# Kernel optimization log

Measured on AMD Instinct MI355X. Metric: run time of the kernel, lower is better.

Reference implementation:

```python
import jax, jax.numpy as jnp
import numpy as np


def setup_inputs() -> dict:
    key = jax.random.key(0)
    ks = jax.random.split(key, 5)
    b, l, ns, ni, d = 128, 64, 32, 16, 256
    scale = 1.0 / np.sqrt(d)
    return {
        "token_features": jax.random.normal(ks[0], (b, l, d), jnp.float32),
        "w_route_ws": jax.random.normal(ks[1], (l, ns, d), jnp.float32) * scale,
        "w_pose_ws": jax.random.normal(ks[2], (l, ns, d, d), jnp.float32) * scale,
        "w_route_si": jax.random.normal(ks[3], (ns, ni, d), jnp.float32) * scale,
        "w_pose_si": jax.random.normal(ks[4], (ns, ni, d, d), jnp.float32) * scale,
    }


def reference(token_features, w_route_ws, w_pose_ws, w_route_si, w_pose_si):
    d_model = token_features.shape[-1]

    # ---- route words -> slots ----
    # token activations ('norm' strategy): mean over d_model -> (b, l)
    a_words = jnp.sum(token_features, axis=-1) / d_model
    # routing logits (b, l, n_slot_caps), softmax over slot caps
    c_ws = jax.nn.softmax(jnp.einsum('lnj,blj->bln', w_route_ws, token_features), axis=-1)
    weighted_c = jnp.einsum('bls,bl->bs', c_ws, a_words)            # (b, ns)
    a_slots = weighted_c / jnp.sum(a_words, axis=-1, keepdims=True)  # (b, ns)
    # pose votes (b, l, ns, d) then weighted aggregation + divisive normalization
    u_hat_slots = jnp.einsum('lnij,blj->blni', w_pose_ws, token_features)
    u_slots = jnp.einsum('bls,bl,blsk->bsk', c_ws, a_words, u_hat_slots) / weighted_c[:, :, None]

    # ---- route slots -> intents ----
    c_si = jax.nn.softmax(jnp.einsum('sij,bsj->bsi', w_route_si, u_slots), axis=-1)
    weighted_c2 = jnp.einsum('bsi,bs->bi', c_si, a_slots)            # (b, ni)
    a_intents = weighted_c2 / jnp.sum(a_slots, axis=-1, keepdims=True)
    u_hat_intents = jnp.einsum('sijk,bsk->bsik', w_pose_si, u_slots)  # (b, ns, ni, d)
    u_intents = jnp.einsum('bsi,bs,bsik->bik', c_si, a_slots, u_hat_intents) / weighted_c2[:, :, None]

    return a_slots, u_slots, a_intents, u_intents
```

## Files before the change

### kernel.cpp

```cpp
#include <hip/hip_runtime.h>
#include <math.h>

#define B  128
#define L  64
#define NS 32
#define NI 16
#define D  256

typedef __attribute__((ext_vector_type(8))) short bf16x8;
typedef __attribute__((ext_vector_type(4))) float f32x4;

__device__ __forceinline__ float wave_reduce_sum(float v) {
#pragma unroll
  for (int off = 32; off; off >>= 1) v += __shfl_xor(v, off, 64);
  return v;
}
__device__ __forceinline__ float wave_reduce_max(float v) {
#pragma unroll
  for (int off = 32; off; off >>= 1) v = fmaxf(v, __shfl_xor(v, off, 64));
  return v;
}

__device__ __forceinline__ ushort bf16_rtne(float f) {
  unsigned u = __float_as_uint(f);
  unsigned r = 0x7FFFu + ((u >> 16) & 1u);
  return (ushort)((u + r) >> 16);
}
__device__ __forceinline__ void split2(float x, ushort& hi, ushort& lo) {
  ushort h = bf16_rtne(x);
  float hf = __uint_as_float(((unsigned)h) << 16);
  hi = h;
  lo = bf16_rtne(x - hf);
}

__global__ __launch_bounds__(256) void k1_route_words(
    const float* __restrict__ tf, const float* __restrict__ wr,
    float* __restrict__ wls, float* __restrict__ a_words) {
  int bl = blockIdx.x;
  int l  = bl & (L - 1);
  int t  = threadIdx.x;
  int wave = t >> 6, lane = t & 63;
  __shared__ float sx[D];
  __shared__ float slog[NS];
  __shared__ float s_aw;
  sx[t] = tf[bl * D + t];
  __syncthreads();
  const float* wbase = wr + l * NS * D;
#pragma unroll
  for (int r = 0; r < 8; ++r) {
    int n = wave * 8 + r;
    const float* w = wbase + n * D;
    float p = 0.f;
#pragma unroll
    for (int jj = 0; jj < 4; ++jj) {
      int j = lane + jj * 64;
      p = fmaf(w[j], sx[j], p);
    }
    p = wave_reduce_sum(p);
    if (lane == 0) slog[n] = p;
  }
  if (wave == 0) {
    float p = sx[lane] + sx[lane + 64] + sx[lane + 128] + sx[lane + 192];
    p = wave_reduce_sum(p);
    if (lane == 0) s_aw = p * (1.f / D);
  }
  __syncthreads();
  if (wave == 0) {
    float aw = s_aw;
    float v = (lane < NS) ? slog[lane] : -INFINITY;
    float m = wave_reduce_max(v);
    float e = (lane < NS) ? __expf(v - m) : 0.f;
    float s = wave_reduce_sum(e);
    if (lane < NS) wls[bl * NS + lane] = (e / s) * aw;
    if (lane == 0) a_words[bl] = aw;
  }
}

__global__ __launch_bounds__(64) void k2_slots_agg(
    const float* __restrict__ wls, const float* __restrict__ a_words,
    float* __restrict__ weighted_c, float* __restrict__ a_slots) {
  int b = blockIdx.x;
  int lane = threadIdx.x;
  float aw = a_words[b * L + lane];
  float sa = wave_reduce_sum(aw);
  if (lane < NS) {
    float wc = 0.f;
    for (int l = 0; l < L; ++l) wc += wls[(b * L + l) * NS + lane];
    weighted_c[b * NS + lane] = wc;
    a_slots[b * NS + lane] = wc / sa;
  }
}

#define BM 128
#define BN 128
#define KC 64
#define KP 72

__global__ __launch_bounds__(256) void k3_mfma(
    const float* __restrict__ tf, const float* __restrict__ wp,
    const float* __restrict__ wls, float* __restrict__ part, int nsplit) {
  __shared__ ushort Ah[BM][KP], Al[BM][KP], Wh[BN][KP], Wl[BN][KP];
  __shared__ float sw[BM];

  int bx   = blockIdx.x;
  int sp   = bx % nsplit;
  int rest = bx / nsplit;
  int it   = rest & 1;
  int s    = rest >> 1;
  int i0   = it * BN;
  int lchunk = L / nsplit;
  int l0     = sp * lchunk;

  int t    = threadIdx.x;
  int jq   = (t & 15) * 4;
  int rb   = t >> 4;
  int lane = t & 63;
  int w    = t >> 6;
  int wm   = w >> 1, wn = w & 1;
  int arow = wm * 64 + (lane & 15);
  int brow = wn * 64 + (lane & 15);
  int ko   = (lane >> 4) * 8;

  f32x4 acc[4][4];
#pragma unroll
  for (int i = 0; i < 4; ++i)
#pragma unroll
    for (int j = 0; j < 4; ++j) acc[i][j] = (f32x4)0.f;

  for (int li = 0; li < lchunk; ++li) {
    int l = l0 + li;
    __syncthreads();
    if (t < BM) sw[t] = wls[((size_t)t * L + l) * NS + s];
    __syncthreads();
    const float* wbase = wp + (size_t)(l * NS + s) * (D * D);
    for (int jc = 0; jc < D; jc += KC) {
      if (jc) __syncthreads();
#pragma unroll
      for (int p = 0; p < 8; ++p) {
        int bb = p * 16 + rb;
        const float4 v = *(const float4*)(tf + ((size_t)bb * L + l) * D + jc + jq);
        float sc = sw[bb];
        ushort4 h4, l4;
        split2(v.x * sc, h4.x, l4.x);
        split2(v.y * sc, h4.y, l4.y);
        split2(v.z * sc, h4.z, l4.z);
        split2(v.w * sc, h4.w, l4.w);
        *(ushort4*)&Ah[bb][jq] = h4;
        *(ushort4*)&Al[bb][jq] = l4;
      }
#pragma unroll
      for (int p = 0; p < 8; ++p) {
        int ii = p * 16 + rb;
        const float4 v = *(const float4*)(wbase + (size_t)(i0 + ii) * D + jc + jq);
        ushort4 h4, l4;
        split2(v.x, h4.x, l4.x);
        split2(v.y, h4.y, l4.y);
        split2(v.z, h4.z, l4.z);
        split2(v.w, h4.w, l4.w);
        *(ushort4*)&Wh[ii][jq] = h4;
        *(ushort4*)&Wl[ii][jq] = l4;
      }
      __syncthreads();
#pragma unroll
      for (int k32 = 0; k32 < 2; ++k32) {
        int kb = k32 * 32 + ko;
        bf16x8 ah[4], av[4], bh[4], bv[4];
#pragma unroll
        for (int mi = 0; mi < 4; ++mi) {
          ah[mi] = *(const bf16x8*)&Ah[arow + mi * 16][kb];
          av[mi] = *(const bf16x8*)&Al[arow + mi * 16][kb];
        }
#pragma unroll
        for (int ni = 0; ni < 4; ++ni) {
          bh[ni] = *(const bf16x8*)&Wh[brow + ni * 16][kb];
          bv[ni] = *(const bf16x8*)&Wl[brow + ni * 16][kb];
        }
#pragma unroll
        for (int mi = 0; mi < 4; ++mi)
#pragma unroll
          for (int ni = 0; ni < 4; ++ni) {
            acc[mi][ni] = __builtin_amdgcn_mfma_f32_16x16x32_bf16(
                ah[mi], bh[ni], acc[mi][ni], 0, 0, 0);
            acc[mi][ni] = __builtin_amdgcn_mfma_f32_16x16x32_bf16(
                ah[mi], bv[ni], acc[mi][ni], 0, 0, 0);
            acc[mi][ni] = __builtin_amdgcn_mfma_f32_16x16x32_bf16(
                av[mi], bh[ni], acc[mi][ni], 0, 0, 0);
          }
      }
    }
  }
  float* pout = part + (((size_t)sp * NS + s) * B) * D + i0;
#pragma unroll
  for (int mi = 0; mi < 4; ++mi)
#pragma unroll
    for (int ni = 0; ni < 4; ++ni) {
      int col = wn * 64 + ni * 16 + (lane & 15);
#pragma unroll
      for (int r = 0; r < 4; ++r) {
        int bb = wm * 64 + mi * 16 + (lane >> 4) * 4 + r;
        pout[(size_t)bb * D + col] = acc[mi][ni][r];
      }
    }
}

__global__ __launch_bounds__(256) void k3r_reduce(
    const float* __restrict__ part, const float* __restrict__ wc,
    float* __restrict__ u_slots, int nsplit) {
  int idx = blockIdx.x * 256 + threadIdx.x;
  int i  = idx & (D - 1);
  int sb = idx >> 8;
  int b  = sb & (B - 1);
  int s  = sb >> 7;
  float v = 0.f;
  for (int sp = 0; sp < nsplit; ++sp)
    v += part[(size_t)sp * (NS * B * D) + idx];
  u_slots[((size_t)b * NS + s) * D + i] = v / wc[b * NS + s];
}

__global__ __launch_bounds__(64) void k4_route_si(
    const float* __restrict__ u_slots, const float* __restrict__ wr_si,
    const float* __restrict__ a_slots, float* __restrict__ w2) {
  int bs = blockIdx.x;
  int s  = bs & (NS - 1);
  int lane = threadIdx.x;
  __shared__ float su[D];
  __shared__ float slog[NI];
#pragma unroll
  for (int jj = 0; jj < 4; ++jj) su[lane + jj * 64] = u_slots[bs * D + lane + jj * 64];
  __syncthreads();
  for (int i = 0; i < NI; ++i) {
    const float* w = wr_si + (s * NI + i) * D;
    float p = 0.f;
#pragma unroll
    for (int jj = 0; jj < 4; ++jj) {
      int j = lane + jj * 64;
      p = fmaf(w[j], su[j], p);
    }
    p = wave_reduce_sum(p);
    if (lane == 0) slog[i] = p;
  }
  __syncthreads();
  float v = (lane < NI) ? slog[lane] : -INFINITY;
  float m = wave_reduce_max(v);
  float e = (lane < NI) ? __expf(v - m) : 0.f;
  float ssum = wave_reduce_sum(e);
  if (lane < NI) w2[bs * NI + lane] = (e / ssum) * a_slots[bs];
}

__global__ __launch_bounds__(64) void k5_intents_agg(
    const float* __restrict__ w2, const float* __restrict__ a_slots,
    float* __restrict__ wc2, float* __restrict__ a_intents) {
  int b = blockIdx.x;
  int lane = threadIdx.x;
  float as = (lane < NS) ? a_slots[b * NS + lane] : 0.f;
  float sas = wave_reduce_sum(as);
  if (lane < NI) {
    float wc = 0.f;
    for (int s = 0; s < NS; ++s) wc += w2[(b * NS + s) * NI + lane];
    wc2[b * NI + lane] = wc;
    a_intents[b * NI + lane] = wc / sas;
  }
}

__global__ __launch_bounds__(256) void k6_wsum(
    const float* __restrict__ wps, float* __restrict__ wsum) {
  __shared__ float red[4][D];
  int si = blockIdx.x;
  int t  = threadIdx.x;
  int k4 = (t & 63) * 4;
  int jg = t >> 6;
  const float* base = wps + (size_t)si * D * D;
  float4 acc = {0.f, 0.f, 0.f, 0.f};
  for (int j = jg; j < D; j += 4) {
    float4 v = *(const float4*)(base + (size_t)j * D + k4);
    acc.x += v.x; acc.y += v.y; acc.z += v.z; acc.w += v.w;
  }
  *(float4*)&red[jg][k4] = acc;
  __syncthreads();
  wsum[si * D + t] = (red[0][t] + red[1][t]) + (red[2][t] + red[3][t]);
}

__global__ __launch_bounds__(256) void k7_uintents(
    const float* __restrict__ u_slots, const float* __restrict__ w2,
    const float* __restrict__ wsum, const float* __restrict__ wc2,
    float* __restrict__ u_intents) {
  int bi = blockIdx.x;
  int b = bi >> 4, i = bi & (NI - 1);
  int k = threadIdx.x;
  float acc = 0.f;
  for (int s = 0; s < NS; ++s) {
    float w = w2[(b * NS + s) * NI + i];
    acc = fmaf(w * u_slots[(b * NS + s) * D + k], wsum[(s * NI + i) * D + k], acc);
  }
  u_intents[bi * D + k] = acc / wc2[bi];
}

extern "C" void kernel_launch(void* const* d_in, const int* in_sizes, int n_in,
                              void* d_out, int out_size, void* d_ws, size_t ws_size,
                              hipStream_t stream) {
  const float* tf    = (const float*)d_in[0];
  const float* wr_ws = (const float*)d_in[1];
  const float* wp_ws = (const float*)d_in[2];
  const float* wr_si = (const float*)d_in[3];
  const float* wp_si = (const float*)d_in[4];

  float* out       = (float*)d_out;
  float* a_slots   = out;
  float* u_slots   = a_slots + B * NS;
  float* a_intents = u_slots + B * NS * D;
  float* u_intents = a_intents + B * NI;

  float* ws         = (float*)d_ws;
  float* wls        = ws;
  float* a_words    = wls + B * L * NS;
  float* weighted_c = a_words + B * L;
  float* w2         = weighted_c + B * NS;
  float* wc2        = w2 + B * NS * NI;
  float* wsum       = wc2 + B * NI;
  float* part       = wsum + NS * NI * D;

  const size_t base_f  = 473088;
  const size_t chunk_f = (size_t)NS * B * D;
  size_t avail_f = ws_size / sizeof(float);
  int nsplit = 1;
  if (avail_f >= base_f + 8 * chunk_f)      nsplit = 8;
  else if (avail_f >= base_f + 4 * chunk_f) nsplit = 4;
  else if (avail_f >= base_f + 2 * chunk_f) nsplit = 2;

  k1_route_words<<<B * L, 256, 0, stream>>>(tf, wr_ws, wls, a_words);
  k2_slots_agg<<<B, 64, 0, stream>>>(wls, a_words, weighted_c, a_slots);
  k3_mfma<<<64 * nsplit, 256, 0, stream>>>(tf, wp_ws, wls, part, nsplit);
  k3r_reduce<<<(NS * B * D) / 256, 256, 0, stream>>>(part, weighted_c, u_slots, nsplit);
  k6_wsum<<<NS * NI, 256, 0, stream>>>(wp_si, wsum);
  k4_route_si<<<B * NS, 64, 0, stream>>>(u_slots, wr_si, a_slots, w2);
  k5_intents_agg<<<B, 64, 0, stream>>>(w2, a_slots, wc2, a_intents);
  k7_uintents<<<B * NI, 256, 0, stream>>>(u_slots, w2, wsum, wc2, u_intents);
}
```

Measured before the change: 270.4 us.

## Fuse wsum reduction into MFMA kernel with register-prefetched pipelined tiles

Merges the w_pose_si column-sum kernel into the main MFMA GEMM launch as extra blocks, so the two independent jobs run side by side. The GEMM tile shrinks from 128x128 with K=64 to 128x64 with K=32, and global loads for the next step are prefetched into registers while the current tile is computed. Routing weights are stored transposed so each block reads its per-slot scales with coalesced loads. The split-L factor is capped at 4. Smaller tiles mean more blocks and more synchronisations per unit of work, and re-reading token features across the four column tiles adds memory traffic.

```diff
diff --git a/kernel.cpp b/kernel.cpp
--- a/kernel.cpp
+++ b/kernel.cpp
@@ -35,8 +35,9 @@
 
 __global__ __launch_bounds__(256) void k1_route_words(
     const float* __restrict__ tf, const float* __restrict__ wr,
-    float* __restrict__ wls, float* __restrict__ a_words) {
+    float* __restrict__ wlsT, float* __restrict__ a_words) {
   int bl = blockIdx.x;
+  int b  = bl >> 6;
   int l  = bl & (L - 1);
   int t  = threadIdx.x;
   int wave = t >> 6, lane = t & 63;
@@ -71,13 +72,13 @@
     float m = wave_reduce_max(v);
     float e = (lane < NS) ? __expf(v - m) : 0.f;
     float s = wave_reduce_sum(e);
-    if (lane < NS) wls[bl * NS + lane] = (e / s) * aw;
+    if (lane < NS) wlsT[(l * NS + lane) * B + b] = (e / s) * aw;
     if (lane == 0) a_words[bl] = aw;
   }
 }
 
 __global__ __launch_bounds__(64) void k2_slots_agg(
-    const float* __restrict__ wls, const float* __restrict__ a_words,
+    const float* __restrict__ wlsT, const float* __restrict__ a_words,
     float* __restrict__ weighted_c, float* __restrict__ a_slots) {
   int b = blockIdx.x;
   int lane = threadIdx.x;
@@ -85,116 +86,148 @@
   float sa = wave_reduce_sum(aw);
   if (lane < NS) {
     float wc = 0.f;
-    for (int l = 0; l < L; ++l) wc += wls[(b * L + l) * NS + lane];
+    for (int l = 0; l < L; ++l) wc += wlsT[(l * NS + lane) * B + b];
     weighted_c[b * NS + lane] = wc;
     a_slots[b * NS + lane] = wc / sa;
   }
 }
 
-#define BM 128
-#define BN 128
-#define KC 64
-#define KP 72
-
-__global__ __launch_bounds__(256) void k3_mfma(
+#define KP 40
+
+__global__ __launch_bounds__(256) void fused_main(
     const float* __restrict__ tf, const float* __restrict__ wp,
-    const float* __restrict__ wls, float* __restrict__ part, int nsplit) {
-  __shared__ ushort Ah[BM][KP], Al[BM][KP], Wh[BN][KP], Wl[BN][KP];
-  __shared__ float sw[BM];
-
-  int bx   = blockIdx.x;
-  int sp   = bx % nsplit;
-  int rest = bx / nsplit;
-  int it   = rest & 1;
-  int s    = rest >> 1;
-  int i0   = it * BN;
+    const float* __restrict__ wlsT, const float* __restrict__ wps,
+    float* __restrict__ part, float* __restrict__ wsum, int nsplit) {
+  union Smem {
+    struct {
+      ushort Ah[128][KP], Al[128][KP];
+      ushort Wh[64][KP],  Wl[64][KP];
+      float  sw[16][128];
+    } k3;
+    struct { float red[4][D]; } k6;
+  };
+  __shared__ Smem sm;
+
+  int bx = blockIdx.x;
+  int t  = threadIdx.x;
+
+  if (bx < NS * NI) {
+    int si = bx;
+    int k4 = (t & 63) * 4;
+    int jg = t >> 6;
+    const float* base = wps + (size_t)si * D * D;
+    float4 acc = {0.f, 0.f, 0.f, 0.f};
+    for (int j = jg; j < D; j += 4) {
+      float4 v = *(const float4*)(base + (size_t)j * D + k4);
+      acc.x += v.x; acc.y += v.y; acc.z += v.z; acc.w += v.w;
+    }
+    *(float4*)&sm.k6.red[jg][k4] = acc;
+    __syncthreads();
+    wsum[si * D + t] = (sm.k6.red[0][t] + sm.k6.red[1][t]) +
+                       (sm.k6.red[2][t] + sm.k6.red[3][t]);
+    return;
+  }
+
+  int kb  = bx - NS * NI;
+  int sp  = kb % nsplit;
+  int rem = kb / nsplit;
+  int it  = rem & 3;
+  int s   = rem >> 2;
+  int i0  = it * 64;
   int lchunk = L / nsplit;
   int l0     = sp * lchunk;
-
-  int t    = threadIdx.x;
-  int jq   = (t & 15) * 4;
-  int rb   = t >> 4;
+  int tot    = lchunk * 8;
+
+  int q8   = (t & 7) * 4;
+  int r32  = t >> 3;
   int lane = t & 63;
-  int w    = t >> 6;
-  int wm   = w >> 1, wn = w & 1;
-  int arow = wm * 64 + (lane & 15);
-  int brow = wn * 64 + (lane & 15);
+  int wv   = t >> 6;
+  int wm   = wv >> 1, wn = wv & 1;
+  int fr   = lane & 15;
   int ko   = (lane >> 4) * 8;
 
-  f32x4 acc[4][4];
-#pragma unroll
-  for (int i = 0; i < 4; ++i)
-#pragma unroll
-    for (int j = 0; j < 4; ++j) acc[i][j] = (f32x4)0.f;
-
-  for (int li = 0; li < lchunk; ++li) {
-    int l = l0 + li;
+  f32x4 acc[4][2];
+#pragma unroll
+  for (int mi = 0; mi < 4; ++mi)
+#pragma unroll
+    for (int ni = 0; ni < 2; ++ni) acc[mi][ni] = (f32x4)0.f;
+
+  float4 rA[4], rW[2];
+  auto load_step = [&](int step) {
+    if (step >= tot) step = tot - 1;
+    int l  = l0 + (step >> 3);
+    int jc = (step & 7) * 32;
+#pragma unroll
+    for (int p = 0; p < 4; ++p)
+      rA[p] = *(const float4*)(tf + ((size_t)(r32 + 32 * p) * L + l) * D + jc + q8);
+    const float* wbase = wp + ((size_t)l * NS + s) * (D * D) + jc + q8;
+#pragma unroll
+    for (int p = 0; p < 2; ++p)
+      rW[p] = *(const float4*)(wbase + (size_t)(i0 + r32 + 32 * p) * D);
+  };
+
+  load_step(0);
+
+  for (int lc = 0; lc < lchunk; lc += 16) {
+    for (int ofs = t; ofs < 16 * 128; ofs += 256) {
+      int li = ofs >> 7, b = ofs & 127;
+      sm.k3.sw[li][b] = wlsT[((size_t)(l0 + lc + li) * NS + s) * B + b];
+    }
     __syncthreads();
-    if (t < BM) sw[t] = wls[((size_t)t * L + l) * NS + s];
-    __syncthreads();
-    const float* wbase = wp + (size_t)(l * NS + s) * (D * D);
-    for (int jc = 0; jc < D; jc += KC) {
-      if (jc) __syncthreads();
-#pragma unroll
-      for (int p = 0; p < 8; ++p) {
-        int bb = p * 16 + rb;
-        const float4 v = *(const float4*)(tf + ((size_t)bb * L + l) * D + jc + jq);
-        float sc = sw[bb];
+    int nst = (lchunk - lc < 16 ? lchunk - lc : 16) * 8;
+    for (int st = 0; st < nst; ++st) {
+      int step = lc * 8 + st;
+      int li   = (step >> 3) - lc;
+#pragma unroll
+      for (int p = 0; p < 4; ++p) {
+        int row = r32 + 32 * p;
+        float sc = sm.k3.sw[li][row];
         ushort4 h4, l4;
-        split2(v.x * sc, h4.x, l4.x);
-        split2(v.y * sc, h4.y, l4.y);
-        split2(v.z * sc, h4.z, l4.z);
-        split2(v.w * sc, h4.w, l4.w);
-        *(ushort4*)&Ah[bb][jq] = h4;
-        *(ushort4*)&Al[bb][jq] = l4;
+        split2(rA[p].x * sc, h4.x, l4.x);
+        split2(rA[p].y * sc, h4.y, l4.y);
+        split2(rA[p].z * sc, h4.z, l4.z);
+        split2(rA[p].w * sc, h4.w, l4.w);
+        *(ushort4*)&sm.k3.Ah[row][q8] = h4;
+        *(ushort4*)&sm.k3.Al[row][q8] = l4;
       }
 #pragma unroll
-      for (int p = 0; p < 8; ++p) {
-        int ii = p * 16 + rb;
-        const float4 v = *(const float4*)(wbase + (size_t)(i0 + ii) * D + jc + jq);
+      for (int p = 0; p < 2; ++p) {
+        int row = r32 + 32 * p;
         ushort4 h4, l4;
-        split2(v.x, h4.x, l4.x);
-        split2(v.y, h4.y, l4.y);
-        split2(v.z, h4.z, l4.z);
-        split2(v.w, h4.w, l4.w);
-        *(ushort4*)&Wh[ii][jq] = h4;
-        *(ushort4*)&Wl[ii][jq] = l4;
+        split2(rW[p].x, h4.x, l4.x);
+        split2(rW[p].y, h4.y, l4.y);
+        split2(rW[p].z, h4.z, l4.z);
+        split2(rW[p].w, h4.w, l4.w);
+        *(ushort4*)&sm.k3.Wh[row][q8] = h4;
+        *(ushort4*)&sm.k3.Wl[row][q8] = l4;
+      }
+      load_step(step + 1);
+      __syncthreads();
+      bf16x8 bh0 = *(const bf16x8*)&sm.k3.Wh[wn * 32 + fr][ko];
+      bf16x8 bl0 = *(const bf16x8*)&sm.k3.Wl[wn * 32 + fr][ko];
+      bf16x8 bh1 = *(const bf16x8*)&sm.k3.Wh[wn * 32 + 16 + fr][ko];
+      bf16x8 bl1 = *(const bf16x8*)&sm.k3.Wl[wn * 32 + 16 + fr][ko];
+#pragma unroll
+      for (int mi = 0; mi < 4; ++mi) {
+        bf16x8 ah = *(const bf16x8*)&sm.k3.Ah[wm * 64 + mi * 16 + fr][ko];
+        bf16x8 al = *(const bf16x8*)&sm.k3.Al[wm * 64 + mi * 16 + fr][ko];
+        acc[mi][0] = __builtin_amdgcn_mfma_f32_16x16x32_bf16(ah, bh0, acc[mi][0], 0, 0, 0);
+        acc[mi][0] = __builtin_amdgcn_mfma_f32_16x16x32_bf16(ah, bl0, acc[mi][0], 0, 0, 0);
+        acc[mi][0] = __builtin_amdgcn_mfma_f32_16x16x32_bf16(al, bh0, acc[mi][0], 0, 0, 0);
+        acc[mi][1] = __builtin_amdgcn_mfma_f32_16x16x32_bf16(ah, bh1, acc[mi][1], 0, 0, 0);
+        acc[mi][1] = __builtin_amdgcn_mfma_f32_16x16x32_bf16(ah, bl1, acc[mi][1], 0, 0, 0);
+        acc[mi][1] = __builtin_amdgcn_mfma_f32_16x16x32_bf16(al, bh1, acc[mi][1], 0, 0, 0);
       }
       __syncthreads();
-#pragma unroll
-      for (int k32 = 0; k32 < 2; ++k32) {
-        int kb = k32 * 32 + ko;
-        bf16x8 ah[4], av[4], bh[4], bv[4];
-#pragma unroll
-        for (int mi = 0; mi < 4; ++mi) {
-          ah[mi] = *(const bf16x8*)&Ah[arow + mi * 16][kb];
-          av[mi] = *(const bf16x8*)&Al[arow + mi * 16][kb];
-        }
-#pragma unroll
-        for (int ni = 0; ni < 4; ++ni) {
-          bh[ni] = *(const bf16x8*)&Wh[brow + ni * 16][kb];
-          bv[ni] = *(const bf16x8*)&Wl[brow + ni * 16][kb];
-        }
-#pragma unroll
-        for (int mi = 0; mi < 4; ++mi)
-#pragma unroll
-          for (int ni = 0; ni < 4; ++ni) {
-            acc[mi][ni] = __builtin_amdgcn_mfma_f32_16x16x32_bf16(
-                ah[mi], bh[ni], acc[mi][ni], 0, 0, 0);
-            acc[mi][ni] = __builtin_amdgcn_mfma_f32_16x16x32_bf16(
-                ah[mi], bv[ni], acc[mi][ni], 0, 0, 0);
-            acc[mi][ni] = __builtin_amdgcn_mfma_f32_16x16x32_bf16(
-                av[mi], bh[ni], acc[mi][ni], 0, 0, 0);
-          }
-      }
-    }
-  }
-  float* pout = part + (((size_t)sp * NS + s) * B) * D + i0;
+    }
+  }
+
+  float* pout = part + ((size_t)sp * NS + s) * (B * D);
 #pragma unroll
   for (int mi = 0; mi < 4; ++mi)
 #pragma unroll
-    for (int ni = 0; ni < 4; ++ni) {
-      int col = wn * 64 + ni * 16 + (lane & 15);
+    for (int ni = 0; ni < 2; ++ni) {
+      int col = i0 + wn * 32 + ni * 16 + fr;
 #pragma unroll
       for (int r = 0; r < 4; ++r) {
         int bb = wm * 64 + mi * 16 + (lane >> 4) * 4 + r;
@@ -262,24 +295,6 @@
   }
 }
 
-__global__ __launch_bounds__(256) void k6_wsum(
-    const float* __restrict__ wps, float* __restrict__ wsum) {
-  __shared__ float red[4][D];
-  int si = blockIdx.x;
-  int t  = threadIdx.x;
-  int k4 = (t & 63) * 4;
-  int jg = t >> 6;
-  const float* base = wps + (size_t)si * D * D;
-  float4 acc = {0.f, 0.f, 0.f, 0.f};
-  for (int j = jg; j < D; j += 4) {
-    float4 v = *(const float4*)(base + (size_t)j * D + k4);
-    acc.x += v.x; acc.y += v.y; acc.z += v.z; acc.w += v.w;
-  }
-  *(float4*)&red[jg][k4] = acc;
-  __syncthreads();
-  wsum[si * D + t] = (red[0][t] + red[1][t]) + (red[2][t] + red[3][t]);
-}
-
 __global__ __launch_bounds__(256) void k7_uintents(
     const float* __restrict__ u_slots, const float* __restrict__ w2,
     const float* __restrict__ wsum, const float* __restrict__ wc2,
@@ -311,8 +326,8 @@
   float* u_intents = a_intents + B * NI;
 
   float* ws         = (float*)d_ws;
-  float* wls        = ws;
-  float* a_words    = wls + B * L * NS;
+  float* wlsT       = ws;
+  float* a_words    = wlsT + L * NS * B;
   float* weighted_c = a_words + B * L;
   float* w2         = weighted_c + B * NS;
   float* wc2        = w2 + B * NS * NI;
@@ -323,15 +338,14 @@
   const size_t chunk_f = (size_t)NS * B * D;
   size_t avail_f = ws_size / sizeof(float);
   int nsplit = 1;
-  if (avail_f >= base_f + 8 * chunk_f)      nsplit = 8;
-  else if (avail_f >= base_f + 4 * chunk_f) nsplit = 4;
+  if (avail_f >= base_f + 4 * chunk_f)      nsplit = 4;
   else if (avail_f >= base_f + 2 * chunk_f) nsplit = 2;
 
-  k1_route_words<<<B * L, 256, 0, stream>>>(tf, wr_ws, wls, a_words);
-  k2_slots_agg<<<B, 64, 0, stream>>>(wls, a_words, weighted_c, a_slots);
-  k3_mfma<<<64 * nsplit, 256, 0, stream>>>(tf, wp_ws, wls, part, nsplit);
+  k1_route_words<<<B * L, 256, 0, stream>>>(tf, wr_ws, wlsT, a_words);
+  k2_slots_agg<<<B, 64, 0, stream>>>(wlsT, a_words, weighted_c, a_slots);
+  fused_main<<<NS * NI + NS * 4 * nsplit, 256, 0, stream>>>(
+      tf, wp_ws, wlsT, wp_si, part, wsum, nsplit);
   k3r_reduce<<<(NS * B * D) / 256, 256, 0, stream>>>(part, weighted_c, u_slots, nsplit);
-  k6_wsum<<<NS * NI, 256, 0, stream>>>(wp_si, wsum);
   k4_route_si<<<B * NS, 64, 0, stream>>>(u_slots, wr_si, a_slots, w2);
   k5_intents_agg<<<B, 64, 0, stream>>>(w2, a_slots, wc2, a_intents);
   k7_uintents<<<B * NI, 256, 0, stream>>>(u_slots, w2, wsum, wc2, u_intents);
```

Result: slower. 494.5 us (+82.9%).
